# Optimization experiments

Hardware: AMD Instinct MI355X
Metric: run time of the kernel (lower is better)

The kernel has to match this reference:

```python
import jax, jax.numpy as jnp
import numpy as np

B, IN, OUT, NUM_F = 131072, 128, 128, 8


def setup_inputs() -> dict:
    key = jax.random.key(0)
    ks = jax.random.split(key, 6)
    x = jax.random.normal(ks[0], (B, IN), dtype=jnp.float32)
    grid = jnp.arange(NUM_F, dtype=jnp.float32) + 1.0            # nn.Parameter(arange(num_f)+1)
    base_weight = jax.random.normal(ks[1], (OUT, IN), dtype=jnp.float32) * 0.05
    scale_sp = jnp.ones((OUT,), dtype=jnp.float32)
    coef = jax.random.uniform(ks[2], (IN, NUM_F), dtype=jnp.float32)  # torch.rand
    # Conv1d(in=IN*NUM_F, out=OUT*NUM_F, k=1, groups=NUM_F) == per-frequency [OUT, IN] matmul
    fan_in = IN  # per-group in-channels * kernel_size(1)
    bound = 1.0 / np.sqrt(fan_in)
    conv_w = jax.random.uniform(ks[3], (NUM_F, OUT, IN), dtype=jnp.float32,
                                minval=-bound, maxval=bound)
    conv_b = jax.random.uniform(ks[4], (NUM_F, OUT), dtype=jnp.float32,
                                minval=-bound, maxval=bound)
    return {"x": x, "grid": grid, "base_weight": base_weight,
            "scale_sp": scale_sp, "coef": coef, "conv_w": conv_w, "conv_b": conv_b}


def reference(x, grid, base_weight, scale_sp, coef, conv_w, conv_b):
    # base path: SiLU(x) @ W_base^T  -> [B, OUT]
    base_out = jax.nn.silu(x) @ base_weight.T
    # Fourier basis: sin(grid_f * x_i) -> [B, F, I]
    s = jnp.sin(x[:, None, :] * grid[None, :, None])
    # coef [I, F] broadcast-multiplied per (i, f)
    s = s * coef.T[None, :, :]                      # [B, F, I]
    # grouped 1x1 conv == per-frequency matmul, plus per-(f, o) bias
    spline = jnp.einsum('bfi,foi->bfo', s, conv_w) + conv_b[None, :, :]  # [B, F, OUT]
    spline_out = spline.sum(axis=1) * scale_sp      # [B, OUT]
    return base_out + spline_out
```

## Files before the change

### kernel.cpp

```cpp
#include <hip/hip_runtime.h>
#include <stdint.h>

#define NCHUNK 9
#define IN_DIM 128
#define OUT_DIM 128
#define NUM_F 8
#define B_TOTAL 131072

#define WBASE_ELEMS (OUT_DIM * IN_DIM)
#define WSIN_ELEMS (8 * OUT_DIM * IN_DIM)
#define SG_SLICE 32768

typedef __bf16 bf16x8 __attribute__((ext_vector_type(8)));
typedef float floatx16 __attribute__((ext_vector_type(16)));

typedef __attribute__((address_space(1))) const unsigned int gas_u32;
typedef __attribute__((address_space(3))) unsigned int las_u32;

__device__ __forceinline__ unsigned short f2bf_rn(float f) {
  unsigned u = __builtin_bit_cast(unsigned, f);
  u += 0x7FFFu + ((u >> 16) & 1u);
  return (unsigned short)(u >> 16);
}

__global__ void skan_prep(const float* __restrict__ base_w,
                          const float* __restrict__ scale_sp,
                          const float* __restrict__ coef,
                          const float* __restrict__ conv_w,
                          const float* __restrict__ conv_b,
                          unsigned short* __restrict__ Wbase,
                          unsigned short* __restrict__ Wsin,
                          float* __restrict__ bias) {
  int b = blockIdx.x;
  int i = threadIdx.x;
  int j = i & 7, q2 = (i >> 3) & 1;
  if (b < NCHUNK * OUT_DIM) {
    int c = b >> 7;
    int o = b & 127;
    if (c == 0) {
      float v = base_w[o * IN_DIM + i];
      int s = i >> 4;
      Wbase[(s * 2 + q2) * 1024 + o * 8 + j] = f2bf_rn(v);
    } else {
      int f = c - 1;
      float v = conv_w[(f * OUT_DIM + o) * IN_DIM + i] * coef[i * NUM_F + f] * scale_sp[o];
      int sg = i >> 5, s2 = (i >> 4) & 1;
      Wsin[((sg * 8 + f) * 4 + s2 * 2 + q2) * 1024 + o * 8 + j] = f2bf_rn(v);
    }
  } else {
    float s = 0.f;
#pragma unroll
    for (int f = 0; f < NUM_F; ++f) s += conv_b[f * OUT_DIM + i];
    bias[i] = s * scale_sp[i];
  }
}

__device__ __forceinline__ unsigned pack2(float lo, float hi) {
  unsigned ulo = __builtin_bit_cast(unsigned, lo) + 0x8000u;
  unsigned uhi = __builtin_bit_cast(unsigned, hi) + 0x8000u;
  return __builtin_amdgcn_perm(uhi, ulo, 0x07060302u);
}

__device__ __forceinline__ bf16x8 pack_frag(const float* v) {
  union { unsigned u[4]; bf16x8 f; } r;
  r.u[0] = pack2(v[0], v[1]);
  r.u[1] = pack2(v[2], v[3]);
  r.u[2] = pack2(v[4], v[5]);
  r.u[3] = pack2(v[6], v[7]);
  return r.f;
}

__device__ __forceinline__ float silu(float v) {
  return v * __builtin_amdgcn_rcpf(1.f + __expf(-v));
}

__global__ __launch_bounds__(256, 2)
void skan_main(const float* __restrict__ x,
               const unsigned short* __restrict__ Wbase,
               const unsigned short* __restrict__ Wsin,
               const float* __restrict__ bias,
               float* __restrict__ out) {
  __shared__ unsigned short sB[SG_SLICE];

  const int tid  = threadIdx.x;
  const int lane = tid & 63;
  const int w    = tid >> 6;
  const int m    = lane & 31;
  const int q2   = lane >> 5;
  const int rowBase = blockIdx.x * 256 + w * 64;

  const int fragCol = m * 8;

  floatx16 acc[2][4];
#pragma unroll
  for (int mt = 0; mt < 2; ++mt)
#pragma unroll
    for (int nt = 0; nt < 4; ++nt)
#pragma unroll
      for (int e = 0; e < 16; ++e) acc[mt][nt][e] = 0.f;

  const float* xr0 = x + (size_t)(rowBase + m) * IN_DIM;
  const float* xr1 = xr0 + 32 * IN_DIM;

#pragma unroll 1
  for (int sg = 0; sg < 4; ++sg) {
    {
      const char* src = (const char*)(Wsin + sg * SG_SLICE);
      char* dst = (char*)sB;
      int off = tid * 16;
#pragma unroll
      for (int it = 0; it < 16; ++it) {
        __builtin_amdgcn_global_load_lds((gas_u32*)(src + off), (las_u32*)(dst + off),
                                         16, 0, 0);
        off += 4096;
      }
    }

    float xv[2][2][8];
#pragma unroll
    for (int mt = 0; mt < 2; ++mt) {
      const float* xr = mt ? xr1 : xr0;
#pragma unroll
      for (int s2 = 0; s2 < 2; ++s2) {
        float4 a = *(const float4*)(xr + sg * 32 + s2 * 16 + q2 * 8);
        float4 b = *(const float4*)(xr + sg * 32 + s2 * 16 + q2 * 8 + 4);
        xv[mt][s2][0] = a.x; xv[mt][s2][1] = a.y;
        xv[mt][s2][2] = a.z; xv[mt][s2][3] = a.w;
        xv[mt][s2][4] = b.x; xv[mt][s2][5] = b.y;
        xv[mt][s2][6] = b.z; xv[mt][s2][7] = b.w;
      }
    }

#pragma unroll
    for (int s2 = 0; s2 < 2; ++s2) {
      int4 Bb[4];
#pragma unroll
      for (int nt = 0; nt < 4; ++nt)
        Bb[nt] = *(const int4*)(Wbase + ((sg * 2 + s2) * 2 + q2) * 1024 +
                                nt * 256 + fragCol);
      float sv[16];
#pragma unroll
      for (int mt = 0; mt < 2; ++mt)
#pragma unroll
        for (int j = 0; j < 8; ++j) sv[mt * 8 + j] = silu(xv[mt][s2][j]);
      bf16x8 a0 = pack_frag(&sv[0]);
      bf16x8 a1 = pack_frag(&sv[8]);
#pragma unroll
      for (int nt = 0; nt < 4; ++nt) {
        bf16x8 bf = __builtin_bit_cast(bf16x8, Bb[nt]);
        acc[0][nt] = __builtin_amdgcn_mfma_f32_32x32x16_bf16(a0, bf, acc[0][nt], 0, 0, 0);
        acc[1][nt] = __builtin_amdgcn_mfma_f32_32x32x16_bf16(a1, bf, acc[1][nt], 0, 0, 0);
      }
    }

    __syncthreads();

#pragma unroll
    for (int s2 = 0; s2 < 2; ++s2) {
      float sp[16], spp[16], c2[16];
#pragma unroll
      for (int mt = 0; mt < 2; ++mt)
#pragma unroll
        for (int j = 0; j < 8; ++j) {
          int v = mt * 8 + j;
          float xx = xv[mt][s2][j];
          sp[v]  = __sinf(xx);
          c2[v]  = 2.f * __cosf(xx);
          spp[v] = 0.f;
        }

#pragma unroll
      for (int c = 1; c <= 8; ++c) {
        bf16x8 Bf[4];
        const unsigned short* bp = sB + ((c - 1) * 4 + s2 * 2 + q2) * 1024 + fragCol;
#pragma unroll
        for (int nt = 0; nt < 4; ++nt)
          Bf[nt] = *(const bf16x8*)(bp + nt * 256);

        if (c >= 2) {
#pragma unroll
          for (int v = 0; v < 16; ++v) {
            float t = __builtin_fmaf(c2[v], sp[v], -spp[v]);
            spp[v] = sp[v];
            sp[v] = t;
          }
        }
        bf16x8 a0 = pack_frag(&sp[0]);
        bf16x8 a1 = pack_frag(&sp[8]);
#pragma unroll
        for (int nt = 0; nt < 4; ++nt) {
          acc[0][nt] = __builtin_amdgcn_mfma_f32_32x32x16_bf16(a0, Bf[nt], acc[0][nt], 0, 0, 0);
          acc[1][nt] = __builtin_amdgcn_mfma_f32_32x32x16_bf16(a1, Bf[nt], acc[1][nt], 0, 0, 0);
        }
      }
    }

    __syncthreads();
  }

#pragma unroll
  for (int mt = 0; mt < 2; ++mt) {
    float* obase = out + (size_t)(rowBase + mt * 32) * OUT_DIM + m;
#pragma unroll
    for (int nt = 0; nt < 4; ++nt) {
      float bv = bias[nt * 32 + m];
#pragma unroll
      for (int e = 0; e < 16; ++e) {
        int rl = (e & 3) + 8 * (e >> 2) + 4 * q2;
        obase[(size_t)rl * OUT_DIM + nt * 32] = acc[mt][nt][e] + bv;
      }
    }
  }
}

extern "C" void kernel_launch(void* const* d_in, const int* in_sizes, int n_in,
                              void* d_out, int out_size, void* d_ws, size_t ws_size,
                              hipStream_t stream) {
  const float* x      = (const float*)d_in[0];
  const float* base_w = (const float*)d_in[2];
  const float* scale  = (const float*)d_in[3];
  const float* coef   = (const float*)d_in[4];
  const float* conv_w = (const float*)d_in[5];
  const float* conv_b = (const float*)d_in[6];

  unsigned short* Wbase = (unsigned short*)d_ws;
  unsigned short* Wsin  = Wbase + WBASE_ELEMS;
  float* bias = (float*)(Wsin + WSIN_ELEMS);
  float* out  = (float*)d_out;

  skan_prep<<<NCHUNK * OUT_DIM + 1, 128, 0, stream>>>(base_w, scale, coef,
                                                      conv_w, conv_b, Wbase, Wsin, bias);
  skan_main<<<B_TOTAL / 256, 256, 0, stream>>>(x, Wbase, Wsin, bias, out);
}
```

Measured before the change: 147.5 us.

## Halve block size and LDS slice, stage sin weights in 8 smaller K-groups

Blocks shrink from 256 to 128 threads (two waves, 128 rows each), and the sin-weight LDS slice drops from 64KB to 32KB. The K loop becomes 8 stages of 16 input channels instead of 4 stages of 32, with the prep-kernel layout changed to match. The aim is more resident blocks per CU, giving more overlap of LDS loads with compute. The trade-off is twice as many LDS fills and barriers per block, and each weight slice is reused across fewer rows. Bf16 packing also switches to the hardware cvt_pk_bf16_f32 instruction when that builtin is available.

```diff
diff --git a/kernel.cpp b/kernel.cpp
--- a/kernel.cpp
+++ b/kernel.cpp
@@ -9,7 +9,8 @@
 
 #define WBASE_ELEMS (OUT_DIM * IN_DIM)
 #define WSIN_ELEMS (8 * OUT_DIM * IN_DIM)
-#define SG_SLICE 32768
+#define NSG 8
+#define SG_SLICE 16384
 
 typedef __bf16 bf16x8 __attribute__((ext_vector_type(8)));
 typedef float floatx16 __attribute__((ext_vector_type(16)));
@@ -39,13 +40,12 @@
     int o = b & 127;
     if (c == 0) {
       float v = base_w[o * IN_DIM + i];
-      int s = i >> 4;
-      Wbase[(s * 2 + q2) * 1024 + o * 8 + j] = f2bf_rn(v);
+      Wbase[((i >> 4) * 2 + q2) * 1024 + o * 8 + j] = f2bf_rn(v);
     } else {
       int f = c - 1;
       float v = conv_w[(f * OUT_DIM + o) * IN_DIM + i] * coef[i * NUM_F + f] * scale_sp[o];
-      int sg = i >> 5, s2 = (i >> 4) & 1;
-      Wsin[((sg * 8 + f) * 4 + s2 * 2 + q2) * 1024 + o * 8 + j] = f2bf_rn(v);
+      int sg = i >> 4;
+      Wsin[sg * SG_SLICE + (f * 2 + q2) * 1024 + o * 8 + j] = f2bf_rn(v);
     }
   } else {
     float s = 0.f;
@@ -56,9 +56,14 @@
 }
 
 __device__ __forceinline__ unsigned pack2(float lo, float hi) {
+#if __has_builtin(__builtin_amdgcn_cvt_pk_bf16_f32)
+  auto r = __builtin_amdgcn_cvt_pk_bf16_f32(lo, hi);
+  return __builtin_bit_cast(unsigned, r);
+#else
   unsigned ulo = __builtin_bit_cast(unsigned, lo) + 0x8000u;
   unsigned uhi = __builtin_bit_cast(unsigned, hi) + 0x8000u;
   return __builtin_amdgcn_perm(uhi, ulo, 0x07060302u);
+#endif
 }
 
 __device__ __forceinline__ bf16x8 pack_frag(const float* v) {
@@ -74,7 +79,7 @@
   return v * __builtin_amdgcn_rcpf(1.f + __expf(-v));
 }
 
-__global__ __launch_bounds__(256, 2)
+__global__ __launch_bounds__(128, 2)
 void skan_main(const float* __restrict__ x,
                const unsigned short* __restrict__ Wbase,
                const unsigned short* __restrict__ Wsin,
@@ -87,7 +92,7 @@
   const int w    = tid >> 6;
   const int m    = lane & 31;
   const int q2   = lane >> 5;
-  const int rowBase = blockIdx.x * 256 + w * 64;
+  const int rowBase = blockIdx.x * 128 + w * 64;
 
   const int fragCol = m * 8;
 
@@ -103,7 +108,7 @@
   const float* xr1 = xr0 + 32 * IN_DIM;
 
 #pragma unroll 1
-  for (int sg = 0; sg < 4; ++sg) {
+  for (int sg = 0; sg < NSG; ++sg) {
     {
       const char* src = (const char*)(Wsin + sg * SG_SLICE);
       char* dst = (char*)sB;
@@ -112,37 +117,30 @@
       for (int it = 0; it < 16; ++it) {
         __builtin_amdgcn_global_load_lds((gas_u32*)(src + off), (las_u32*)(dst + off),
                                          16, 0, 0);
-        off += 4096;
-      }
-    }
-
-    float xv[2][2][8];
+        off += 2048;
+      }
+    }
+
+    float xv[2][8];
 #pragma unroll
     for (int mt = 0; mt < 2; ++mt) {
       const float* xr = mt ? xr1 : xr0;
-#pragma unroll
-      for (int s2 = 0; s2 < 2; ++s2) {
-        float4 a = *(const float4*)(xr + sg * 32 + s2 * 16 + q2 * 8);
-        float4 b = *(const float4*)(xr + sg * 32 + s2 * 16 + q2 * 8 + 4);
-        xv[mt][s2][0] = a.x; xv[mt][s2][1] = a.y;
-        xv[mt][s2][2] = a.z; xv[mt][s2][3] = a.w;
-        xv[mt][s2][4] = b.x; xv[mt][s2][5] = b.y;
-        xv[mt][s2][6] = b.z; xv[mt][s2][7] = b.w;
-      }
-    }
-
-#pragma unroll
-    for (int s2 = 0; s2 < 2; ++s2) {
+      float4 a = *(const float4*)(xr + sg * 16 + q2 * 8);
+      float4 b = *(const float4*)(xr + sg * 16 + q2 * 8 + 4);
+      xv[mt][0] = a.x; xv[mt][1] = a.y; xv[mt][2] = a.z; xv[mt][3] = a.w;
+      xv[mt][4] = b.x; xv[mt][5] = b.y; xv[mt][6] = b.z; xv[mt][7] = b.w;
+    }
+
+    {
       int4 Bb[4];
 #pragma unroll
       for (int nt = 0; nt < 4; ++nt)
-        Bb[nt] = *(const int4*)(Wbase + ((sg * 2 + s2) * 2 + q2) * 1024 +
-                                nt * 256 + fragCol);
+        Bb[nt] = *(const int4*)(Wbase + (sg * 2 + q2) * 1024 + nt * 256 + fragCol);
       float sv[16];
 #pragma unroll
       for (int mt = 0; mt < 2; ++mt)
 #pragma unroll
-        for (int j = 0; j < 8; ++j) sv[mt * 8 + j] = silu(xv[mt][s2][j]);
+        for (int j = 0; j < 8; ++j) sv[mt * 8 + j] = silu(xv[mt][j]);
       bf16x8 a0 = pack_frag(&sv[0]);
       bf16x8 a1 = pack_frag(&sv[8]);
 #pragma unroll
@@ -155,43 +153,40 @@
 
     __syncthreads();
 
-#pragma unroll
-    for (int s2 = 0; s2 < 2; ++s2) {
-      float sp[16], spp[16], c2[16];
-#pragma unroll
-      for (int mt = 0; mt < 2; ++mt)
-#pragma unroll
-        for (int j = 0; j < 8; ++j) {
-          int v = mt * 8 + j;
-          float xx = xv[mt][s2][j];
-          sp[v]  = __sinf(xx);
-          c2[v]  = 2.f * __cosf(xx);
-          spp[v] = 0.f;
+    float sp[16], spp[16], c2[16];
+#pragma unroll
+    for (int mt = 0; mt < 2; ++mt)
+#pragma unroll
+      for (int j = 0; j < 8; ++j) {
+        int v = mt * 8 + j;
+        float xx = xv[mt][j];
+        sp[v]  = __sinf(xx);
+        c2[v]  = 2.f * __cosf(xx);
+        spp[v] = 0.f;
+      }
+
+#pragma unroll
+    for (int c = 1; c <= 8; ++c) {
+      bf16x8 Bf[4];
+      const unsigned short* bp = sB + ((c - 1) * 2 + q2) * 1024 + fragCol;
+#pragma unroll
+      for (int nt = 0; nt < 4; ++nt)
+        Bf[nt] = *(const bf16x8*)(bp + nt * 256);
+
+      if (c >= 2) {
+#pragma unroll
+        for (int v = 0; v < 16; ++v) {
+          float t = __builtin_fmaf(c2[v], sp[v], -spp[v]);
+          spp[v] = sp[v];
+          sp[v] = t;
         }
-
-#pragma unroll
-      for (int c = 1; c <= 8; ++c) {
-        bf16x8 Bf[4];
-        const unsigned short* bp = sB + ((c - 1) * 4 + s2 * 2 + q2) * 1024 + fragCol;
-#pragma unroll
-        for (int nt = 0; nt < 4; ++nt)
-          Bf[nt] = *(const bf16x8*)(bp + nt * 256);
-
-        if (c >= 2) {
-#pragma unroll
-          for (int v = 0; v < 16; ++v) {
-            float t = __builtin_fmaf(c2[v], sp[v], -spp[v]);
-            spp[v] = sp[v];
-            sp[v] = t;
-          }
-        }
-        bf16x8 a0 = pack_frag(&sp[0]);
-        bf16x8 a1 = pack_frag(&sp[8]);
-#pragma unroll
-        for (int nt = 0; nt < 4; ++nt) {
-          acc[0][nt] = __builtin_amdgcn_mfma_f32_32x32x16_bf16(a0, Bf[nt], acc[0][nt], 0, 0, 0);
-          acc[1][nt] = __builtin_amdgcn_mfma_f32_32x32x16_bf16(a1, Bf[nt], acc[1][nt], 0, 0, 0);
-        }
+      }
+      bf16x8 a0 = pack_frag(&sp[0]);
+      bf16x8 a1 = pack_frag(&sp[8]);
+#pragma unroll
+      for (int nt = 0; nt < 4; ++nt) {
+        acc[0][nt] = __builtin_amdgcn_mfma_f32_32x32x16_bf16(a0, Bf[nt], acc[0][nt], 0, 0, 0);
+        acc[1][nt] = __builtin_amdgcn_mfma_f32_32x32x16_bf16(a1, Bf[nt], acc[1][nt], 0, 0, 0);
       }
     }
 
@@ -230,5 +225,5 @@
 
   skan_prep<<<NCHUNK * OUT_DIM + 1, 128, 0, stream>>>(base_w, scale, coef,
                                                       conv_w, conv_b, Wbase, Wsin, bias);
-  skan_main<<<B_TOTAL / 256, 256, 0, stream>>>(x, Wbase, Wsin, bias, out);
-}
+  skan_main<<<B_TOTAL / 128, 128, 0, stream>>>(x, Wbase, Wsin, bias, out);
+}
```

Result: slower. 152.8 us (+3.6%).
